# Performance work log

Hardware: AMD Instinct MI355X
Metric: run time of the kernel (lower is better)

The kernel has to match this reference:

```python
import jax, jax.numpy as jnp
import numpy as np

N_HEAD, D_MODEL, D_HEAD = 16, 1024, 64
QLEN, BSZ, RLEN = 2048, 2, 2048
SCALE = 1.0 / (D_HEAD ** 0.5)


def setup_inputs() -> dict:
    key = jax.random.key(0)
    ks = jax.random.split(key, 7)
    return {
        "w": jax.random.normal(ks[0], (QLEN, BSZ, D_MODEL), dtype=jnp.float32),
        "r": jax.random.normal(ks[1], (RLEN, D_MODEL), dtype=jnp.float32),
        "qkv_w": jax.random.normal(ks[2], (D_MODEL, 3 * N_HEAD * D_HEAD), dtype=jnp.float32) * 0.02,
        "r_net_w": jax.random.normal(ks[3], (D_MODEL, N_HEAD * D_HEAD), dtype=jnp.float32) * 0.02,
        "o_w": jax.random.normal(ks[4], (N_HEAD * D_HEAD, D_MODEL), dtype=jnp.float32) * 0.02,
        "r_r_bias": jax.random.normal(ks[5], (N_HEAD, D_HEAD), dtype=jnp.float32) * 0.02,
        "r_w_bias": jax.random.normal(ks[6], (N_HEAD, D_HEAD), dtype=jnp.float32) * 0.02,
    }


def _rel_shift(x):
    # x: [qlen, rlen, bsz, n_head]
    q, r, b, n = x.shape
    x = jnp.pad(x, ((0, 0), (1, 0), (0, 0), (0, 0)))
    x = x.reshape(r + 1, q, b, n)[1:]
    return x.reshape(q, r, b, n)


def reference(w, r, qkv_w, r_net_w, o_w, r_r_bias, r_w_bias):
    qlen, bsz, _ = w.shape
    rlen = r.shape[0]
    # qkv projection: [qlen, bsz, 3*H*D]
    w_heads = jnp.einsum('ibm,mh->ibh', w, qkv_w)
    w_head_q, w_head_k, w_head_v = jnp.split(w_heads, 3, axis=-1)
    klen = w_head_k.shape[0]
    w_head_q = w_head_q.reshape(qlen, bsz, N_HEAD, D_HEAD)
    w_head_k = w_head_k.reshape(klen, bsz, N_HEAD, D_HEAD)
    w_head_v = w_head_v.reshape(klen, bsz, N_HEAD, D_HEAD)
    # relative position keys: [rlen, H, D]
    r_head_k = jnp.einsum('jm,mh->jh', r, r_net_w).reshape(rlen, N_HEAD, D_HEAD)

    rw_head_q = w_head_q + r_w_bias  # content bias
    rr_head_q = w_head_q + r_r_bias  # position bias
    AC = jnp.einsum('ibnd,jbnd->ijbn', rw_head_q, w_head_k)
    BD = jnp.einsum('ibnd,jnd->ijbn', rr_head_q, r_head_k)
    BD = _rel_shift(BD)[:, :klen]

    attn_score = (AC + BD) * SCALE
    attn_prob = jax.nn.softmax(attn_score, axis=1)  # over klen axis
    attn_vec = jnp.einsum('ijbn,jbnd->ibnd', attn_prob, w_head_v)
    attn_vec = attn_vec.reshape(qlen, bsz, N_HEAD * D_HEAD)
    attn_out = jnp.einsum('ibh,hm->ibm', attn_vec, o_w)
    return (w + attn_out, attn_prob, AC, BD)
```

## Files before the change

kernel.cpp:

```cpp
#include <hip/hip_runtime.h>
#include <hip/hip_bf16.h>


typedef unsigned short u16;
typedef __attribute__((ext_vector_type(8))) short short8;
typedef __attribute__((ext_vector_type(4))) float f32x4;
typedef __attribute__((ext_vector_type(4))) unsigned short u16x4;

__device__ __forceinline__ u16 f2bf(float x){
  unsigned u = __float_as_uint(x);
  u += 0x7fffu + ((u >> 16) & 1u);
  return (u16)(u >> 16);
}
__device__ __forceinline__ float bf2f(u16 s){
  return __uint_as_float(((unsigned)s) << 16);
}
__device__ __forceinline__ f32x4 mfma16(short8 a, short8 b, f32x4 c){
  return __builtin_amdgcn_mfma_f32_16x16x32_bf16(a, b, c, 0, 0, 0);
}


__global__ __launch_bounds__(256) void k_cast(const float* __restrict__ src, u16* __restrict__ dst, int n4){
  int i = blockIdx.x * 256 + threadIdx.x;
  if (i >= n4) return;
  f32x4 v = *(const f32x4*)(src + (size_t)i * 4);
  u16x4 o;
  #pragma unroll
  for (int q = 0; q < 4; ++q) o[q] = f2bf(v[q]);
  *(u16x4*)(dst + (size_t)i * 4) = o;
}

__global__ __launch_bounds__(256) void k_tc(const float* __restrict__ src, u16* __restrict__ dst, int R, int C){
  __shared__ float ld[32][33];
  int c0 = blockIdx.x * 32, r0 = blockIdx.y * 32;
  int t = threadIdx.x;
  int r = t >> 3, c4 = (t & 7) * 4;
  f32x4 v = *(const f32x4*)(src + (size_t)(r0 + r) * C + c0 + c4);
  #pragma unroll
  for (int q = 0; q < 4; ++q) ld[r][c4 + q] = v[q];
  __syncthreads();
  int c = t >> 3, r4 = (t & 7) * 4;
  u16x4 o;
  #pragma unroll
  for (int q = 0; q < 4; ++q) o[q] = f2bf(ld[r4 + q][c]);
  *(u16x4*)(dst + (size_t)(c0 + c) * R + r0 + r4) = o;
}


template<int MODE>
__global__ __launch_bounds__(512) void k_gemm(const u16* __restrict__ A, const u16* __restrict__ Bt,
        u16* __restrict__ o0, u16* __restrict__ o1, u16* __restrict__ o2,
        const float* __restrict__ wres, float* __restrict__ outf)
{
  __shared__ __align__(16) u16 As[128][40];
  __shared__ __align__(16) u16 Bs[256][40];
  const int t = threadIdx.x;
  const int wave = t >> 6, lane = t & 63;
  const int wr = wave >> 2, wc = wave & 3;
  const int g = lane >> 4, li = lane & 15;
  const int m0 = blockIdx.x * 128, n0 = blockIdx.y * 256;
  f32x4 acc[4][4] = {};
  const int ar = t >> 2, ac8 = (t & 3) * 8;
  for (int kt = 0; kt < 32; ++kt){
    int k0 = kt * 32;
    *(short8*)&As[ar][ac8] = *(const short8*)(A + (size_t)(m0 + ar) * 1024 + k0 + ac8);
    #pragma unroll
    for (int u = 0; u < 2; ++u){
      int id = t + 512 * u; int br = id >> 2, bc8 = (id & 3) * 8;
      *(short8*)&Bs[br][bc8] = *(const short8*)(Bt + (size_t)(n0 + br) * 1024 + k0 + bc8);
    }
    __syncthreads();
    short8 af[4], bfv[4];
    #pragma unroll
    for (int mf = 0; mf < 4; ++mf) af[mf] = *(const short8*)&As[wr * 64 + mf * 16 + li][g * 8];
    #pragma unroll
    for (int nf = 0; nf < 4; ++nf) bfv[nf] = *(const short8*)&Bs[wc * 64 + nf * 16 + li][g * 8];
    #pragma unroll
    for (int mf = 0; mf < 4; ++mf)
      #pragma unroll
      for (int nf = 0; nf < 4; ++nf)
        acc[mf][nf] = mfma16(af[mf], bfv[nf], acc[mf][nf]);
    __syncthreads();
  }
  #pragma unroll
  for (int mf = 0; mf < 4; ++mf)
  #pragma unroll
  for (int nf = 0; nf < 4; ++nf)
  #pragma unroll
  for (int r = 0; r < 4; ++r){
    int gr = m0 + wr * 64 + mf * 16 + g * 4 + r;
    int gc = n0 + wc * 64 + nf * 16 + li;
    float v = acc[mf][nf][r];
    if (MODE == 0){
      int part = gc >> 10, hh = gc & 1023;
      int hn = hh >> 6, d = hh & 63;
      int i = gr >> 1, b = gr & 1;
      u16* dst = (part == 0) ? o0 : ((part == 1) ? o1 : o2);
      dst[((((b << 4) + hn) * 2048 + i) << 6) + d] = f2bf(v);
    } else if (MODE == 1){
      int hn = gc >> 6, d = gc & 63;
      o0[((hn * 2048 + gr) << 6) + d] = f2bf(v);
    } else {
      size_t idx = (size_t)gr * 1024 + gc;
      outf[idx] = wres[idx] + v;
    }
  }
}

__global__ __launch_bounds__(256) void k_bias(const u16* __restrict__ Km, const float* __restrict__ bv,
                                              float* __restrict__ out, int total){
  int idx = blockIdx.x * 256 + threadIdx.x;
  if (idx >= total) return;
  int n = (idx >> 11) & 15;
  const u16* kr = Km + ((size_t)idx << 6);
  const float* bp = bv + n * 64;
  float s = 0.f;
  #pragma unroll
  for (int d8 = 0; d8 < 8; ++d8){
    short8 v = *(const short8*)(kr + d8 * 8);
    #pragma unroll
    for (int q = 0; q < 8; ++q) s += bp[d8 * 8 + q] * bf2f((u16)v[q]);
  }
  out[idx] = s;
}

__global__ __launch_bounds__(256) void k_trv(const u16* __restrict__ V, u16* __restrict__ Vt){
  __shared__ __align__(16) u16 ld[64][72];
  int bn = blockIdx.x, j0 = blockIdx.y * 64;
  int t = threadIdx.x;
  #pragma unroll
  for (int u = 0; u < 2; ++u){
    int id = t + 256 * u; int r = id >> 3, c8 = (id & 7) * 8;
    *(short8*)&ld[r][c8] = *(const short8*)(V + ((size_t)(bn * 2048 + j0 + r) << 6) + c8);
  }
  __syncthreads();
  #pragma unroll
  for (int u = 0; u < 2; ++u){
    int id = t + 256 * u; int d = id >> 3, j8 = (id & 7) * 8;
    short8 o;
    #pragma unroll
    for (int q = 0; q < 8; ++q) o[q] = ld[j8 + q][d];
    *(short8*)(Vt + ((size_t)(bn * 64 + d) << 11) + j0 + j8) = o;
  }
}

__global__ __launch_bounds__(512, 4) void k_bd(const u16* __restrict__ Q, const u16* __restrict__ RK,
        const float* __restrict__ bias_bd, float* __restrict__ BD)
{
  __shared__ u16 Cs[32 * 271];
  const int t = threadIdx.x, wave = t >> 6, lane = t & 63;
  const int g = lane >> 4, li = lane & 15;
  const int i0 = blockIdx.x * 16, b = blockIdx.y;
  const int cbase = blockIdx.z * 512;
  short8 qa[2][2];
  #pragma unroll
  for (int nn = 0; nn < 2; ++nn){
    int bn = b * 16 + wave * 2 + nn;
    const u16* qp = Q + ((size_t)(bn * 2048 + i0 + li) << 6) + g * 8;
    qa[nn][0] = *(const short8*)qp;
    qa[nn][1] = *(const short8*)(qp + 32);
  }
  for (int ch = 0; ch < 16; ++ch){
    int c0 = cbase + ch * 32;
    #pragma unroll
    for (int nn = 0; nn < 2; ++nn){
      int n = wave * 2 + nn;
      #pragma unroll
      for (int cf = 0; cf < 2; ++cf){
        int ccol = c0 + cf * 16 + li;
        const u16* rp = RK + ((size_t)(n * 2048 + ccol) << 6) + g * 8;
        short8 b0 = *(const short8*)rp;
        short8 b1 = *(const short8*)(rp + 32);
        f32x4 acc = {};
        acc = mfma16(qa[nn][0], b0, acc);
        acc = mfma16(qa[nn][1], b1, acc);
        float bb = bias_bd[n * 2048 + ccol];
        #pragma unroll
        for (int r = 0; r < 4; ++r)
          Cs[(cf * 16 + li) * 271 + n * 17 + g * 4 + r] = f2bf(acc[r] + bb);
      }
    }
    __syncthreads();
    #pragma unroll
    for (int u = 0; u < 4; ++u){
      int flat4 = t + 512 * u;
      int n4 = (flat4 & 3) * 4, cl = (flat4 >> 2) & 31, row = flat4 >> 7;
      int ip = i0 + row, cg = c0 + cl;
      bool p1 = (cg >= 2047 - ip);
      int ro = p1 ? ip : (ip - 1);
      int j  = cg + (p1 ? (ip - 2047) : (ip + 1));
      if (ro >= 0){
        f32x4 v;
        #pragma unroll
        for (int q = 0; q < 4; ++q) v[q] = bf2f(Cs[cl * 271 + (n4 + q) * 17 + row]);
        *(f32x4*)(BD + (((size_t)ro * 2048 + j) << 5) + b * 16 + n4) = v;
      }
    }
    __syncthreads();
  }
}

__global__ __launch_bounds__(256) void k_bdiag(float* __restrict__ BD){
  int idx = blockIdx.x * 256 + threadIdx.x;
  int i = idx >> 5, c = idx & 31;
  if (i < 2047) BD[(((size_t)i * 2048 + i + 1) << 5) + c] = 0.f;
}

__global__ __launch_bounds__(512, 4) void k_stats(const u16* __restrict__ Q, const u16* __restrict__ Kc,
        const float* __restrict__ bias_ac, const float* __restrict__ BD,
        float* __restrict__ ACo, float* __restrict__ m_part, float* __restrict__ l_part)
{
  __shared__ float sA[16 * 545];
  __shared__ u16  sB[32 * 271];
  const int t = threadIdx.x, wave = t >> 6, lane = t & 63;
  const int g = lane >> 4, li = lane & 15;
  const int i0 = blockIdx.x * 16, b = blockIdx.y;
  const int jbase = blockIdx.z * 512;
  short8 qa[2][2];
  #pragma unroll
  for (int nn = 0; nn < 2; ++nn){
    int bn = b * 16 + wave * 2 + nn;
    const u16* qp = Q + ((size_t)(bn * 2048 + i0 + li) << 6) + g * 8;
    qa[nn][0] = *(const short8*)qp;
    qa[nn][1] = *(const short8*)(qp + 32);
  }
  float m_[2][4], l_[2][4];
  #pragma unroll
  for (int nn = 0; nn < 2; ++nn)
    #pragma unroll
    for (int r = 0; r < 4; ++r){ m_[nn][r] = -__builtin_inff(); l_[nn][r] = 0.f; }

  for (int ch = 0; ch < 16; ++ch){
    int j0 = jbase + ch * 32;
    __syncthreads();
    #pragma unroll
    for (int u = 0; u < 4; ++u){
      int flat4 = t + 512 * u;
      int n4 = (flat4 & 3) * 4, jl = (flat4 >> 2) & 31, row = flat4 >> 7;
      f32x4 v = *(const f32x4*)(BD + (((size_t)(i0 + row) * 2048 + j0 + jl) << 5) + b * 16 + n4);
      #pragma unroll
      for (int q = 0; q < 4; ++q) sA[row * 545 + jl * 17 + n4 + q] = v[q];
    }
    __syncthreads();
    #pragma unroll
    for (int nn = 0; nn < 2; ++nn){
      int n = wave * 2 + nn, bn = b * 16 + n;
      float sv[2][4];
      #pragma unroll
      for (int cf = 0; cf < 2; ++cf){
        int jc = j0 + cf * 16 + li;
        const u16* kp = Kc + ((size_t)(bn * 2048 + jc) << 6) + g * 8;
        short8 b0 = *(const short8*)kp;
        short8 b1 = *(const short8*)(kp + 32);
        f32x4 acc = {};
        acc = mfma16(qa[nn][0], b0, acc);
        acc = mfma16(qa[nn][1], b1, acc);
        float ba = bias_ac[bn * 2048 + jc];
        #pragma unroll
        for (int r = 0; r < 4; ++r){
          float av = acc[r] + ba;
          sB[(cf * 16 + li) * 271 + n * 17 + g * 4 + r] = f2bf(av);
          sv[cf][r] = (av + sA[(g * 4 + r) * 545 + (cf * 16 + li) * 17 + n]) * 0.125f;
        }
      }
      float cm[4], mn[4], ps[4];
      #pragma unroll
      for (int r = 0; r < 4; ++r) cm[r] = fmaxf(sv[0][r], sv[1][r]);
      #pragma unroll
      for (int off = 1; off < 16; off <<= 1)
        #pragma unroll
        for (int r = 0; r < 4; ++r) cm[r] = fmaxf(cm[r], __shfl_xor(cm[r], off));
      #pragma unroll
      for (int r = 0; r < 4; ++r){
        mn[r] = fmaxf(m_[nn][r], cm[r]);
        ps[r] = __expf(sv[0][r] - mn[r]) + __expf(sv[1][r] - mn[r]);
      }
      #pragma unroll
      for (int off = 1; off < 16; off <<= 1)
        #pragma unroll
        for (int r = 0; r < 4; ++r) ps[r] += __shfl_xor(ps[r], off);
      #pragma unroll
      for (int r = 0; r < 4; ++r){
        l_[nn][r] = l_[nn][r] * __expf(m_[nn][r] - mn[r]) + ps[r];
        m_[nn][r] = mn[r];
      }
    }
    __syncthreads();
    #pragma unroll
    for (int u = 0; u < 4; ++u){
      int flat4 = t + 512 * u;
      int n4 = (flat4 & 3) * 4, jl = (flat4 >> 2) & 31, row = flat4 >> 7;
      f32x4 v;
      #pragma unroll
      for (int q = 0; q < 4; ++q) v[q] = bf2f(sB[jl * 271 + (n4 + q) * 17 + row]);
      *(f32x4*)(ACo + (((size_t)(i0 + row) * 2048 + j0 + jl) << 5) + b * 16 + n4) = v;
    }
  }
  if (li == 0){
    #pragma unroll
    for (int nn = 0; nn < 2; ++nn)
      #pragma unroll
      for (int r = 0; r < 4; ++r){
        int bn = b * 16 + wave * 2 + nn;
        size_t o = ((size_t)(blockIdx.z * 32 + bn)) * 2048 + i0 + g * 4 + r;
        m_part[o] = m_[nn][r];
        l_part[o] = l_[nn][r];
      }
  }
}

__global__ __launch_bounds__(256) void k_comb(const float* __restrict__ mp, const float* __restrict__ lp,
                                              float* __restrict__ mf, float* __restrict__ lf){
  int idx = blockIdx.x * 256 + threadIdx.x;
  float m = -__builtin_inff();
  #pragma unroll
  for (int js = 0; js < 4; ++js) m = fmaxf(m, mp[js * 65536 + idx]);
  float l = 0.f;
  #pragma unroll
  for (int js = 0; js < 4; ++js) l += lp[js * 65536 + idx] * __expf(mp[js * 65536 + idx] - m);
  mf[idx] = m;
  lf[idx] = l;
}

__global__ __launch_bounds__(512, 4) void k_prob_pv(const u16* __restrict__ Q, const u16* __restrict__ Kc,
        const u16* __restrict__ Vt, const float* __restrict__ bias_ac, const float* __restrict__ BD,
        const float* __restrict__ m_f, const float* __restrict__ l_f,
        float* __restrict__ PROB, float* __restrict__ Ovp)
{
  __shared__ float sA[16 * 545];
  __shared__ u16  sB[32 * 271];
  const int t = threadIdx.x, wave = t >> 6, lane = t & 63;
  const int g = lane >> 4, li = lane & 15;
  const int i0 = blockIdx.x * 16, b = blockIdx.y;
  const int jbase = blockIdx.z * 512;
  short8 qa[2][2];
  float m_[2][4], rl_[2][4];
  #pragma unroll
  for (int nn = 0; nn < 2; ++nn){
    int bn = b * 16 + wave * 2 + nn;
    const u16* qp = Q + ((size_t)(bn * 2048 + i0 + li) << 6) + g * 8;
    qa[nn][0] = *(const short8*)qp;
    qa[nn][1] = *(const short8*)(qp + 32);
    #pragma unroll
    for (int r = 0; r < 4; ++r){
      m_[nn][r]  = m_f[bn * 2048 + i0 + g * 4 + r];
      rl_[nn][r] = 1.f / l_f[bn * 2048 + i0 + g * 4 + r];
    }
  }
  f32x4 oacc[2][4] = {};

  for (int ch = 0; ch < 16; ++ch){
    int j0 = jbase + ch * 32;
    __syncthreads();
    #pragma unroll
    for (int u = 0; u < 4; ++u){
      int flat4 = t + 512 * u;
      int n4 = (flat4 & 3) * 4, jl = (flat4 >> 2) & 31, row = flat4 >> 7;
      f32x4 v = *(const f32x4*)(BD + (((size_t)(i0 + row) * 2048 + j0 + jl) << 5) + b * 16 + n4);
      #pragma unroll
      for (int q = 0; q < 4; ++q) sA[row * 545 + jl * 17 + n4 + q] = v[q];
    }
    __syncthreads();
    #pragma unroll
    for (int nn = 0; nn < 2; ++nn){
      int n = wave * 2 + nn, bn = b * 16 + n;
      #pragma unroll
      for (int cf = 0; cf < 2; ++cf){
        int jc = j0 + cf * 16 + li;
        const u16* kp = Kc + ((size_t)(bn * 2048 + jc) << 6) + g * 8;
        short8 b0 = *(const short8*)kp;
        short8 b1 = *(const short8*)(kp + 32);
        f32x4 acc = {};
        acc = mfma16(qa[nn][0], b0, acc);
        acc = mfma16(qa[nn][1], b1, acc);
        float ba = bias_ac[bn * 2048 + jc];
        #pragma unroll
        for (int r = 0; r < 4; ++r){
          float s = (acc[r] + ba + sA[(g * 4 + r) * 545 + (cf * 16 + li) * 17 + n]) * 0.125f;
          float p = __expf(s - m_[nn][r]) * rl_[nn][r];
          sB[(cf * 16 + li) * 271 + n * 17 + g * 4 + r] = f2bf(p);
        }
      }
    }
    #pragma unroll
    for (int nn = 0; nn < 2; ++nn){
      int n = wave * 2 + nn, bn = b * 16 + n;
      short8 pa;
      #pragma unroll
      for (int tt = 0; tt < 8; ++tt) pa[tt] = (short)sB[(g * 8 + tt) * 271 + n * 17 + li];
      const u16* vb = Vt + ((size_t)(bn * 64) << 11) + j0 + g * 8;
      #pragma unroll
      for (int vf = 0; vf < 4; ++vf){
        short8 bv = *(const short8*)(vb + ((size_t)(vf * 16 + li) << 11));
        oacc[nn][vf] = mfma16(pa, bv, oacc[nn][vf]);
      }
    }
    __syncthreads();
    #pragma unroll
    for (int u = 0; u < 4; ++u){
      int flat4 = t + 512 * u;
      int n4 = (flat4 & 3) * 4, jl = (flat4 >> 2) & 31, row = flat4 >> 7;
      f32x4 v;
      #pragma unroll
      for (int q = 0; q < 4; ++q) v[q] = bf2f(sB[jl * 271 + (n4 + q) * 17 + row]);
      *(f32x4*)(PROB + (((size_t)(i0 + row) * 2048 + j0 + jl) << 5) + b * 16 + n4) = v;
    }
  }
  float* op = Ovp + (size_t)blockIdx.z * 4194304;
  #pragma unroll
  for (int nn = 0; nn < 2; ++nn){
    int n = wave * 2 + nn;
    #pragma unroll
    for (int vf = 0; vf < 4; ++vf)
      #pragma unroll
      for (int r = 0; r < 4; ++r)
        op[(size_t)((i0 + g * 4 + r) * 2 + b) * 1024 + n * 64 + vf * 16 + li] = oacc[nn][vf][r];
  }
}

__global__ __launch_bounds__(256) void k_ovred(const float* __restrict__ ovp, u16* __restrict__ ov){
  int i = blockIdx.x * 256 + threadIdx.x;
  const f32x4* p = (const f32x4*)ovp;
  f32x4 s = p[i];
  #pragma unroll
  for (int js = 1; js < 4; ++js) s += p[(size_t)js * 1048576 + i];
  u16x4 o;
  #pragma unroll
  for (int q = 0; q < 4; ++q) o[q] = f2bf(s[q]);
  ((u16x4*)ov)[i] = o;
}


extern "C" void kernel_launch(void* const* d_in, const int* in_sizes, int n_in,
                              void* d_out, int out_size, void* d_ws, size_t ws_size,
                              hipStream_t stream)
{
  const float* w      = (const float*)d_in[0];
  const float* r      = (const float*)d_in[1];
  const float* qkv_w  = (const float*)d_in[2];
  const float* rnet_w = (const float*)d_in[3];
  const float* o_w    = (const float*)d_in[4];
  const float* rrb    = (const float*)d_in[5];
  const float* rwb    = (const float*)d_in[6];

  char* ws = (char*)d_ws;
  size_t off = 0;
  auto alloc = [&](size_t bytes) -> void* {
    void* p = ws + off; off += (bytes + 255) & ~(size_t)255; return p;
  };
  u16* Xbf    = (u16*)alloc((size_t)4096 * 1024 * 2);
  u16* Rbf    = (u16*)alloc((size_t)2048 * 1024 * 2);
  u16* Wqkvt  = (u16*)alloc((size_t)3072 * 1024 * 2);
  u16* Wrt    = (u16*)alloc((size_t)1024 * 1024 * 2);
  u16* Wot    = (u16*)alloc((size_t)1024 * 1024 * 2);
  u16* Qs     = (u16*)alloc((size_t)32 * 2048 * 64 * 2);
  u16* Ks     = (u16*)alloc((size_t)32 * 2048 * 64 * 2);
  u16* Vs     = (u16*)alloc((size_t)32 * 2048 * 64 * 2);
  u16* Vts    = (u16*)alloc((size_t)32 * 64 * 2048 * 2);
  u16* RKs    = (u16*)alloc((size_t)16 * 2048 * 64 * 2);
  float* bias_ac = (float*)alloc((size_t)32 * 2048 * 4);
  float* bias_bd = (float*)alloc((size_t)16 * 2048 * 4);
  float* m_part  = (float*)alloc((size_t)4 * 32 * 2048 * 4);
  float* l_part  = (float*)alloc((size_t)4 * 32 * 2048 * 4);
  float* m_fin   = (float*)alloc((size_t)32 * 2048 * 4);
  float* l_fin   = (float*)alloc((size_t)32 * 2048 * 4);
  float* Ovp     = (float*)alloc((size_t)4 * 4096 * 1024 * 4);
  u16* Ov     = (u16*)alloc((size_t)4096 * 1024 * 2);

  float* out0 = (float*)d_out;
  float* PROB = out0 + 4194304;
  float* ACo  = PROB + 134217728;
  float* BDo  = ACo  + 134217728;

  k_cast<<<dim3(4096), dim3(256), 0, stream>>>(w, Xbf, 1048576);
  k_cast<<<dim3(2048), dim3(256), 0, stream>>>(r, Rbf, 524288);
  k_tc<<<dim3(96, 32), dim3(256), 0, stream>>>(qkv_w,  Wqkvt, 1024, 3072);
  k_tc<<<dim3(32, 32), dim3(256), 0, stream>>>(rnet_w, Wrt,   1024, 1024);
  k_tc<<<dim3(32, 32), dim3(256), 0, stream>>>(o_w,    Wot,   1024, 1024);
  k_gemm<0><<<dim3(32, 12), dim3(512), 0, stream>>>(Xbf, Wqkvt, Qs, Ks, Vs, nullptr, nullptr);
  k_gemm<1><<<dim3(16, 4),  dim3(512), 0, stream>>>(Rbf, Wrt,  RKs, nullptr, nullptr, nullptr, nullptr);
  k_bias<<<dim3(256), dim3(256), 0, stream>>>(Ks,  rwb, bias_ac, 65536);
  k_bias<<<dim3(128), dim3(256), 0, stream>>>(RKs, rrb, bias_bd, 32768);
  k_trv<<<dim3(32, 32), dim3(256), 0, stream>>>(Vs, Vts);
  k_bd<<<dim3(128, 2, 4), dim3(512), 0, stream>>>(Qs, RKs, bias_bd, BDo);
  k_bdiag<<<dim3(256), dim3(256), 0, stream>>>(BDo);
  k_stats<<<dim3(128, 2, 4), dim3(512), 0, stream>>>(Qs, Ks, bias_ac, BDo, ACo, m_part, l_part);
  k_comb<<<dim3(256), dim3(256), 0, stream>>>(m_part, l_part, m_fin, l_fin);
  k_prob_pv<<<dim3(128, 2, 4), dim3(512), 0, stream>>>(Qs, Ks, Vts, bias_ac, BDo, m_fin, l_fin, PROB, Ovp);
  k_ovred<<<dim3(4096), dim3(256), 0, stream>>>(Ovp, Ov);
  k_gemm<2><<<dim3(32, 4), dim3(512), 0, stream>>>(Ov, Wot, nullptr, nullptr, nullptr, w, out0);
}
```

Measured before the change: 1.375 ms.

## Fuse rel-shifted BD computation into stats and prob kernels, drop BD round trips

The separate BD kernel and diagonal-zero kernel are removed. The stats and prob/PV kernels now compute the rel-shifted BD tile on the fly: for each tile they run diagonal-band MFMAs with Q rows i and i+1 against the relevant RK columns and scatter the results into shared memory. This avoids writing BD to global memory and reading it back twice, which is 512MB of fp32 traffic. BD is still written once from the stats kernel, and all big outputs now use nontemporal stores. The cost is redundant BD MFMAs in both kernels, extra shared-memory clears each iteration, and BD values rounded to bf16 before they are added into the scores.

Result: slower. 1.614 ms (+17.4%).

```diff
diff --git a/kernel.cpp b/kernel.cpp
--- a/kernel.cpp
+++ b/kernel.cpp
@@ -17,6 +17,9 @@
 }
 __device__ __forceinline__ f32x4 mfma16(short8 a, short8 b, f32x4 c){
   return __builtin_amdgcn_mfma_f32_16x16x32_bf16(a, b, c, 0, 0, 0);
+}
+__device__ __forceinline__ void ntst4(float* p, f32x4 v){
+  __builtin_nontemporal_store(v, (f32x4*)p);
 }
 
 
@@ -144,86 +147,79 @@
   }
 }
 
-__global__ __launch_bounds__(512, 4) void k_bd(const u16* __restrict__ Q, const u16* __restrict__ RK,
-        const float* __restrict__ bias_bd, float* __restrict__ BD)
+__device__ __forceinline__ void bd_scatter(u16* sBD, const u16* __restrict__ RK,
+        const float* __restrict__ bias_bd, const short8 qa[2][2], const short8 qb[2][2],
+        int m, int wave, int g, int li)
 {
-  __shared__ u16 Cs[32 * 271];
+  #pragma unroll
+  for (int nn = 0; nn < 2; ++nn){
+    int n = wave * 2 + nn;
+    #pragma unroll
+    for (int tt = 0; tt < 3; ++tt){
+      int c0 = m + 2032 + tt * 16;
+      if (c0 < 0 || c0 > 2032) continue;
+      const u16* rp = RK + ((size_t)(n * 2048 + c0 + li) << 6) + g * 8;
+      short8 b0 = *(const short8*)rp;
+      short8 b1 = *(const short8*)(rp + 32);
+      f32x4 acc = {};
+      acc = mfma16(qa[nn][0], b0, acc);
+      acc = mfma16(qa[nn][1], b1, acc);
+      float bb = bias_bd[n * 2048 + c0 + li];
+      int off = tt * 16 - 15;
+      #pragma unroll
+      for (int r = 0; r < 4; ++r){
+        int fr = g * 4 + r;
+        int jw = li + fr + off;
+        if ((unsigned)jw < 32u) sBD[fr * 544 + jw * 17 + n] = f2bf(acc[r] + bb);
+      }
+    }
+    #pragma unroll
+    for (int tt = 0; tt < 4; ++tt){
+      int c0 = m - 32 + tt * 16;
+      if (c0 < 0 || c0 > 2032) continue;
+      const u16* rp = RK + ((size_t)(n * 2048 + c0 + li) << 6) + g * 8;
+      short8 b0 = *(const short8*)rp;
+      short8 b1 = *(const short8*)(rp + 32);
+      f32x4 acc = {};
+      acc = mfma16(qb[nn][0], b0, acc);
+      acc = mfma16(qb[nn][1], b1, acc);
+      float bb = bias_bd[n * 2048 + c0 + li];
+      int off = tt * 16 - 30;
+      #pragma unroll
+      for (int r = 0; r < 4; ++r){
+        int fr = g * 4 + r;
+        int jw = li + fr + off;
+        if ((unsigned)jw < 32u) sBD[fr * 544 + jw * 17 + n] = f2bf(acc[r] + bb);
+      }
+    }
+  }
+}
+
+__global__ __launch_bounds__(512, 4) void k_statsF(const u16* __restrict__ Q, const u16* __restrict__ RK,
+        const u16* __restrict__ Kc, const float* __restrict__ bias_ac, const float* __restrict__ bias_bd,
+        float* __restrict__ ACo, float* __restrict__ BDo,
+        float* __restrict__ m_part, float* __restrict__ l_part)
+{
+  __shared__ __align__(16) u16 sBD[16 * 544];
+  __shared__ __align__(16) u16 sAC[32 * 271];
   const int t = threadIdx.x, wave = t >> 6, lane = t & 63;
   const int g = lane >> 4, li = lane & 15;
   const int i0 = blockIdx.x * 16, b = blockIdx.y;
-  const int cbase = blockIdx.z * 512;
-  short8 qa[2][2];
+  const int jbase = blockIdx.z * 512;
+  short8 qa[2][2], qb[2][2];
   #pragma unroll
   for (int nn = 0; nn < 2; ++nn){
     int bn = b * 16 + wave * 2 + nn;
     const u16* qp = Q + ((size_t)(bn * 2048 + i0 + li) << 6) + g * 8;
     qa[nn][0] = *(const short8*)qp;
     qa[nn][1] = *(const short8*)(qp + 32);
-  }
-  for (int ch = 0; ch < 16; ++ch){
-    int c0 = cbase + ch * 32;
-    #pragma unroll
-    for (int nn = 0; nn < 2; ++nn){
-      int n = wave * 2 + nn;
-      #pragma unroll
-      for (int cf = 0; cf < 2; ++cf){
-        int ccol = c0 + cf * 16 + li;
-        const u16* rp = RK + ((size_t)(n * 2048 + ccol) << 6) + g * 8;
-        short8 b0 = *(const short8*)rp;
-        short8 b1 = *(const short8*)(rp + 32);
-        f32x4 acc = {};
-        acc = mfma16(qa[nn][0], b0, acc);
-        acc = mfma16(qa[nn][1], b1, acc);
-        float bb = bias_bd[n * 2048 + ccol];
-        #pragma unroll
-        for (int r = 0; r < 4; ++r)
-          Cs[(cf * 16 + li) * 271 + n * 17 + g * 4 + r] = f2bf(acc[r] + bb);
-      }
-    }
-    __syncthreads();
-    #pragma unroll
-    for (int u = 0; u < 4; ++u){
-      int flat4 = t + 512 * u;
-      int n4 = (flat4 & 3) * 4, cl = (flat4 >> 2) & 31, row = flat4 >> 7;
-      int ip = i0 + row, cg = c0 + cl;
-      bool p1 = (cg >= 2047 - ip);
-      int ro = p1 ? ip : (ip - 1);
-      int j  = cg + (p1 ? (ip - 2047) : (ip + 1));
-      if (ro >= 0){
-        f32x4 v;
-        #pragma unroll
-        for (int q = 0; q < 4; ++q) v[q] = bf2f(Cs[cl * 271 + (n4 + q) * 17 + row]);
-        *(f32x4*)(BD + (((size_t)ro * 2048 + j) << 5) + b * 16 + n4) = v;
-      }
-    }
-    __syncthreads();
-  }
-}
-
-__global__ __launch_bounds__(256) void k_bdiag(float* __restrict__ BD){
-  int idx = blockIdx.x * 256 + threadIdx.x;
-  int i = idx >> 5, c = idx & 31;
-  if (i < 2047) BD[(((size_t)i * 2048 + i + 1) << 5) + c] = 0.f;
-}
-
-__global__ __launch_bounds__(512, 4) void k_stats(const u16* __restrict__ Q, const u16* __restrict__ Kc,
-        const float* __restrict__ bias_ac, const float* __restrict__ BD,
-        float* __restrict__ ACo, float* __restrict__ m_part, float* __restrict__ l_part)
-{
-  __shared__ float sA[16 * 545];
-  __shared__ u16  sB[32 * 271];
-  const int t = threadIdx.x, wave = t >> 6, lane = t & 63;
-  const int g = lane >> 4, li = lane & 15;
-  const int i0 = blockIdx.x * 16, b = blockIdx.y;
-  const int jbase = blockIdx.z * 512;
-  short8 qa[2][2];
-  #pragma unroll
-  for (int nn = 0; nn < 2; ++nn){
-    int bn = b * 16 + wave * 2 + nn;
-    const u16* qp = Q + ((size_t)(bn * 2048 + i0 + li) << 6) + g * 8;
-    qa[nn][0] = *(const short8*)qp;
-    qa[nn][1] = *(const short8*)(qp + 32);
-  }
+    int rowB = i0 + 1 + li; if (rowB > 2047) rowB = 2047;
+    const u16* qp2 = Q + ((size_t)(bn * 2048 + rowB) << 6) + g * 8;
+    qb[nn][0] = *(const short8*)qp2;
+    qb[nn][1] = *(const short8*)(qp2 + 32);
+  }
+  for (int w = t; w < 4352; w += 512) ((unsigned*)sBD)[w] = 0;
+
   float m_[2][4], l_[2][4];
   #pragma unroll
   for (int nn = 0; nn < 2; ++nn)
@@ -232,15 +228,9 @@
 
   for (int ch = 0; ch < 16; ++ch){
     int j0 = jbase + ch * 32;
-    __syncthreads();
-    #pragma unroll
-    for (int u = 0; u < 4; ++u){
-      int flat4 = t + 512 * u;
-      int n4 = (flat4 & 3) * 4, jl = (flat4 >> 2) & 31, row = flat4 >> 7;
-      f32x4 v = *(const f32x4*)(BD + (((size_t)(i0 + row) * 2048 + j0 + jl) << 5) + b * 16 + n4);
-      #pragma unroll
-      for (int q = 0; q < 4; ++q) sA[row * 545 + jl * 17 + n4 + q] = v[q];
-    }
+    int m = j0 - i0;
+    __syncthreads();
+    bd_scatter(sBD, RK, bias_bd, qa, qb, m, wave, g, li);
     __syncthreads();
     #pragma unroll
     for (int nn = 0; nn < 2; ++nn){
@@ -259,8 +249,9 @@
         #pragma unroll
         for (int r = 0; r < 4; ++r){
           float av = acc[r] + ba;
-          sB[(cf * 16 + li) * 271 + n * 17 + g * 4 + r] = f2bf(av);
-          sv[cf][r] = (av + sA[(g * 4 + r) * 545 + (cf * 16 + li) * 17 + n]) * 0.125f;
+          sAC[(cf * 16 + li) * 271 + n * 17 + g * 4 + r] = f2bf(av);
+          float bd = bf2f(sBD[(g * 4 + r) * 544 + (cf * 16 + li) * 17 + n]);
+          sv[cf][r] = (av + bd) * 0.125f;
         }
       }
       float cm[4], mn[4], ps[4];
@@ -285,16 +276,26 @@
         m_[nn][r] = mn[r];
       }
     }
-    __syncthreads();
     #pragma unroll
     for (int u = 0; u < 4; ++u){
       int flat4 = t + 512 * u;
       int n4 = (flat4 & 3) * 4, jl = (flat4 >> 2) & 31, row = flat4 >> 7;
       f32x4 v;
       #pragma unroll
-      for (int q = 0; q < 4; ++q) v[q] = bf2f(sB[jl * 271 + (n4 + q) * 17 + row]);
-      *(f32x4*)(ACo + (((size_t)(i0 + row) * 2048 + j0 + jl) << 5) + b * 16 + n4) = v;
-    }
+      for (int q = 0; q < 4; ++q) v[q] = bf2f(sBD[row * 544 + jl * 17 + n4 + q]);
+      ntst4(BDo + (((size_t)(i0 + row) * 2048 + j0 + jl) << 5) + b * 16 + n4, v);
+    }
+    __syncthreads();
+    #pragma unroll
+    for (int u = 0; u < 4; ++u){
+      int flat4 = t + 512 * u;
+      int n4 = (flat4 & 3) * 4, jl = (flat4 >> 2) & 31, row = flat4 >> 7;
+      f32x4 v;
+      #pragma unroll
+      for (int q = 0; q < 4; ++q) v[q] = bf2f(sAC[jl * 271 + (n4 + q) * 17 + row]);
+      ntst4(ACo + (((size_t)(i0 + row) * 2048 + j0 + jl) << 5) + b * 16 + n4, v);
+    }
+    for (int w = t; w < 4352; w += 512) ((unsigned*)sBD)[w] = 0;
   }
   if (li == 0){
     #pragma unroll
@@ -322,13 +323,14 @@
   lf[idx] = l;
 }
 
-__global__ __launch_bounds__(512, 4) void k_prob_pv(const u16* __restrict__ Q, const u16* __restrict__ Kc,
-        const u16* __restrict__ Vt, const float* __restrict__ bias_ac, const float* __restrict__ BD,
+__global__ __launch_bounds__(512, 4) void k_probF(const u16* __restrict__ Q, const u16* __restrict__ RK,
+        const u16* __restrict__ Kc, const u16* __restrict__ Vt,
+        const float* __restrict__ bias_ac, const float* __restrict__ bias_bd,
         const float* __restrict__ m_f, const float* __restrict__ l_f,
         float* __restrict__ PROB, float* __restrict__ Ovp)
 {
-  __shared__ float sA[16 * 545];
-  __shared__ u16  sB[32 * 271];
+  __shared__ __align__(16) u16 sBD[16 * 544];
+  __shared__ __align__(16) u16 sP[32 * 271];
   const int t = threadIdx.x, wave = t >> 6, lane = t & 63;
   const int g = lane >> 4, li = lane & 15;
   const int i0 = blockIdx.x * 16, b = blockIdx.y;
@@ -347,18 +349,24 @@
       rl_[nn][r] = 1.f / l_f[bn * 2048 + i0 + g * 4 + r];
     }
   }
+  for (int w = t; w < 4352; w += 512) ((unsigned*)sBD)[w] = 0;
   f32x4 oacc[2][4] = {};
 
   for (int ch = 0; ch < 16; ++ch){
     int j0 = jbase + ch * 32;
-    __syncthreads();
-    #pragma unroll
-    for (int u = 0; u < 4; ++u){
-      int flat4 = t + 512 * u;
-      int n4 = (flat4 & 3) * 4, jl = (flat4 >> 2) & 31, row = flat4 >> 7;
-      f32x4 v = *(const f32x4*)(BD + (((size_t)(i0 + row) * 2048 + j0 + jl) << 5) + b * 16 + n4);
-      #pragma unroll
-      for (int q = 0; q < 4; ++q) sA[row * 545 + jl * 17 + n4 + q] = v[q];
+    int m = j0 - i0;
+    __syncthreads();
+    {
+      short8 qb[2][2];
+      #pragma unroll
+      for (int nn = 0; nn < 2; ++nn){
+        int bn = b * 16 + wave * 2 + nn;
+        int rowB = i0 + 1 + li; if (rowB > 2047) rowB = 2047;
+        const u16* qp2 = Q + ((size_t)(bn * 2048 + rowB) << 6) + g * 8;
+        qb[nn][0] = *(const short8*)qp2;
+        qb[nn][1] = *(const short8*)(qp2 + 32);
+      }
+      bd_scatter(sBD, RK, bias_bd, qa, qb, m, wave, g, li);
     }
     __syncthreads();
     #pragma unroll
@@ -376,9 +384,10 @@
         float ba = bias_ac[bn * 2048 + jc];
         #pragma unroll
         for (int r = 0; r < 4; ++r){
-          float s = (acc[r] + ba + sA[(g * 4 + r) * 545 + (cf * 16 + li) * 17 + n]) * 0.125f;
+          float bd = bf2f(sBD[(g * 4 + r) * 544 + (cf * 16 + li) * 17 + n]);
+          float s = (acc[r] + ba + bd) * 0.125f;
           float p = __expf(s - m_[nn][r]) * rl_[nn][r];
-          sB[(cf * 16 + li) * 271 + n * 17 + g * 4 + r] = f2bf(p);
+          sP[(cf * 16 + li) * 271 + n * 17 + g * 4 + r] = f2bf(p);
         }
       }
     }
@@ -387,7 +396,7 @@
       int n = wave * 2 + nn, bn = b * 16 + n;
       short8 pa;
       #pragma unroll
-      for (int tt = 0; tt < 8; ++tt) pa[tt] = (short)sB[(g * 8 + tt) * 271 + n * 17 + li];
+      for (int tt = 0; tt < 8; ++tt) pa[tt] = (short)sP[(g * 8 + tt) * 271 + n * 17 + li];
       const u16* vb = Vt + ((size_t)(bn * 64) << 11) + j0 + g * 8;
       #pragma unroll
       for (int vf = 0; vf < 4; ++vf){
@@ -402,9 +411,10 @@
       int n4 = (flat4 & 3) * 4, jl = (flat4 >> 2) & 31, row = flat4 >> 7;
       f32x4 v;
       #pragma unroll
-      for (int q = 0; q < 4; ++q) v[q] = bf2f(sB[jl * 271 + (n4 + q) * 17 + row]);
-      *(f32x4*)(PROB + (((size_t)(i0 + row) * 2048 + j0 + jl) << 5) + b * 16 + n4) = v;
-    }
+      for (int q = 0; q < 4; ++q) v[q] = bf2f(sP[jl * 271 + (n4 + q) * 17 + row]);
+      ntst4(PROB + (((size_t)(i0 + row) * 2048 + j0 + jl) << 5) + b * 16 + n4, v);
+    }
+    for (int w = t; w < 4352; w += 512) ((unsigned*)sBD)[w] = 0;
   }
   float* op = Ovp + (size_t)blockIdx.z * 4194304;
   #pragma unroll
@@ -482,11 +492,9 @@
   k_bias<<<dim3(256), dim3(256), 0, stream>>>(Ks,  rwb, bias_ac, 65536);
   k_bias<<<dim3(128), dim3(256), 0, stream>>>(RKs, rrb, bias_bd, 32768);
   k_trv<<<dim3(32, 32), dim3(256), 0, stream>>>(Vs, Vts);
-  k_bd<<<dim3(128, 2, 4), dim3(512), 0, stream>>>(Qs, RKs, bias_bd, BDo);
-  k_bdiag<<<dim3(256), dim3(256), 0, stream>>>(BDo);
-  k_stats<<<dim3(128, 2, 4), dim3(512), 0, stream>>>(Qs, Ks, bias_ac, BDo, ACo, m_part, l_part);
+  k_statsF<<<dim3(128, 2, 4), dim3(512), 0, stream>>>(Qs, RKs, Ks, bias_ac, bias_bd, ACo, BDo, m_part, l_part);
   k_comb<<<dim3(256), dim3(256), 0, stream>>>(m_part, l_part, m_fin, l_fin);
-  k_prob_pv<<<dim3(128, 2, 4), dim3(512), 0, stream>>>(Qs, Ks, Vts, bias_ac, BDo, m_fin, l_fin, PROB, Ovp);
+  k_probF<<<dim3(128, 2, 4), dim3(512), 0, stream>>>(Qs, RKs, Ks, Vts, bias_ac, bias_bd, m_fin, l_fin, PROB, Ovp);
   k_ovred<<<dim3(4096), dim3(256), 0, stream>>>(Ovp, Ov);
   k_gemm<2><<<dim3(32, 4), dim3(512), 0, stream>>>(Ov, Wot, nullptr, nullptr, nullptr, w, out0);
 }
```

## Prefetch BD tiles into registers, store BD in LDS as bf16, use nontemporal stores

Applied to the files above, without the earlier changes.

The stats and prob/PV kernels now prefetch the next chunk's BD tile into registers while the current chunk is being processed, so global load latency overlaps compute. The BD tile is staged in shared memory as truncated bf16 with a padded vectorized layout, which cuts LDS size and store traffic. The large BD, AC and PROB output writes use nontemporal stores so these streams do not pollute the cache. The risks are extra register pressure from the prefetch buffers and the precision lost by truncating BD to bf16 in the score calculation.

After: 1.257 ms. -8.5%, faster.

```diff
diff --git a/kernel.cpp b/kernel.cpp
--- a/kernel.cpp
+++ b/kernel.cpp
@@ -17,6 +17,9 @@
 }
 __device__ __forceinline__ f32x4 mfma16(short8 a, short8 b, f32x4 c){
   return __builtin_amdgcn_mfma_f32_16x16x32_bf16(a, b, c, 0, 0, 0);
+}
+__device__ __forceinline__ void ntst4(float* p, f32x4 v){
+  __builtin_nontemporal_store(v, (f32x4*)p);
 }
 
 
@@ -193,7 +196,7 @@
         f32x4 v;
         #pragma unroll
         for (int q = 0; q < 4; ++q) v[q] = bf2f(Cs[cl * 271 + (n4 + q) * 17 + row]);
-        *(f32x4*)(BD + (((size_t)ro * 2048 + j) << 5) + b * 16 + n4) = v;
+        ntst4(BD + (((size_t)ro * 2048 + j) << 5) + b * 16 + n4, v);
       }
     }
     __syncthreads();
@@ -210,8 +213,8 @@
         const float* __restrict__ bias_ac, const float* __restrict__ BD,
         float* __restrict__ ACo, float* __restrict__ m_part, float* __restrict__ l_part)
 {
-  __shared__ float sA[16 * 545];
-  __shared__ u16  sB[32 * 271];
+  __shared__ __align__(16) u16 sA[16 * 648];
+  __shared__ u16 sB[32 * 271];
   const int t = threadIdx.x, wave = t >> 6, lane = t & 63;
   const int g = lane >> 4, li = lane & 15;
   const int i0 = blockIdx.x * 16, b = blockIdx.y;
@@ -230,6 +233,14 @@
     #pragma unroll
     for (int r = 0; r < 4; ++r){ m_[nn][r] = -__builtin_inff(); l_[nn][r] = 0.f; }
 
+  f32x4 pfv[4];
+  #pragma unroll
+  for (int u = 0; u < 4; ++u){
+    int flat4 = t + 512 * u;
+    int n4 = (flat4 & 3) * 4, jl = (flat4 >> 2) & 31, row = flat4 >> 7;
+    pfv[u] = *(const f32x4*)(BD + (((size_t)(i0 + row) * 2048 + jbase + jl) << 5) + b * 16 + n4);
+  }
+
   for (int ch = 0; ch < 16; ++ch){
     int j0 = jbase + ch * 32;
     __syncthreads();
@@ -237,9 +248,18 @@
     for (int u = 0; u < 4; ++u){
       int flat4 = t + 512 * u;
       int n4 = (flat4 & 3) * 4, jl = (flat4 >> 2) & 31, row = flat4 >> 7;
-      f32x4 v = *(const f32x4*)(BD + (((size_t)(i0 + row) * 2048 + j0 + jl) << 5) + b * 16 + n4);
-      #pragma unroll
-      for (int q = 0; q < 4; ++q) sA[row * 545 + jl * 17 + n4 + q] = v[q];
+      u16x4 o;
+      #pragma unroll
+      for (int q = 0; q < 4; ++q) o[q] = (u16)(__float_as_uint(pfv[u][q]) >> 16);
+      *(u16x4*)&sA[row * 648 + jl * 20 + n4] = o;
+    }
+    if (ch + 1 < 16){
+      #pragma unroll
+      for (int u = 0; u < 4; ++u){
+        int flat4 = t + 512 * u;
+        int n4 = (flat4 & 3) * 4, jl = (flat4 >> 2) & 31, row = flat4 >> 7;
+        pfv[u] = *(const f32x4*)(BD + (((size_t)(i0 + row) * 2048 + j0 + 32 + jl) << 5) + b * 16 + n4);
+      }
     }
     __syncthreads();
     #pragma unroll
@@ -260,7 +280,8 @@
         for (int r = 0; r < 4; ++r){
           float av = acc[r] + ba;
           sB[(cf * 16 + li) * 271 + n * 17 + g * 4 + r] = f2bf(av);
-          sv[cf][r] = (av + sA[(g * 4 + r) * 545 + (cf * 16 + li) * 17 + n]) * 0.125f;
+          float bd = bf2f(sA[(g * 4 + r) * 648 + (cf * 16 + li) * 20 + n]);
+          sv[cf][r] = (av + bd) * 0.125f;
         }
       }
       float cm[4], mn[4], ps[4];
@@ -293,7 +314,7 @@
       f32x4 v;
       #pragma unroll
       for (int q = 0; q < 4; ++q) v[q] = bf2f(sB[jl * 271 + (n4 + q) * 17 + row]);
-      *(f32x4*)(ACo + (((size_t)(i0 + row) * 2048 + j0 + jl) << 5) + b * 16 + n4) = v;
+      ntst4(ACo + (((size_t)(i0 + row) * 2048 + j0 + jl) << 5) + b * 16 + n4, v);
     }
   }
   if (li == 0){
@@ -327,8 +348,8 @@
         const float* __restrict__ m_f, const float* __restrict__ l_f,
         float* __restrict__ PROB, float* __restrict__ Ovp)
 {
-  __shared__ float sA[16 * 545];
-  __shared__ u16  sB[32 * 271];
+  __shared__ __align__(16) u16 sA[16 * 648];
+  __shared__ u16 sB[32 * 271];
   const int t = threadIdx.x, wave = t >> 6, lane = t & 63;
   const int g = lane >> 4, li = lane & 15;
   const int i0 = blockIdx.x * 16, b = blockIdx.y;
@@ -349,6 +370,14 @@
   }
   f32x4 oacc[2][4] = {};
 
+  f32x4 pfv[4];
+  #pragma unroll
+  for (int u = 0; u < 4; ++u){
+    int flat4 = t + 512 * u;
+    int n4 = (flat4 & 3) * 4, jl = (flat4 >> 2) & 31, row = flat4 >> 7;
+    pfv[u] = *(const f32x4*)(BD + (((size_t)(i0 + row) * 2048 + jbase + jl) << 5) + b * 16 + n4);
+  }
+
   for (int ch = 0; ch < 16; ++ch){
     int j0 = jbase + ch * 32;
     __syncthreads();
@@ -356,9 +385,18 @@
     for (int u = 0; u < 4; ++u){
       int flat4 = t + 512 * u;
       int n4 = (flat4 & 3) * 4, jl = (flat4 >> 2) & 31, row = flat4 >> 7;
-      f32x4 v = *(const f32x4*)(BD + (((size_t)(i0 + row) * 2048 + j0 + jl) << 5) + b * 16 + n4);
-      #pragma unroll
-      for (int q = 0; q < 4; ++q) sA[row * 545 + jl * 17 + n4 + q] = v[q];
+      u16x4 o;
+      #pragma unroll
+      for (int q = 0; q < 4; ++q) o[q] = (u16)(__float_as_uint(pfv[u][q]) >> 16);
+      *(u16x4*)&sA[row * 648 + jl * 20 + n4] = o;
+    }
+    if (ch + 1 < 16){
+      #pragma unroll
+      for (int u = 0; u < 4; ++u){
+        int flat4 = t + 512 * u;
+        int n4 = (flat4 & 3) * 4, jl = (flat4 >> 2) & 31, row = flat4 >> 7;
+        pfv[u] = *(const f32x4*)(BD + (((size_t)(i0 + row) * 2048 + j0 + 32 + jl) << 5) + b * 16 + n4);
+      }
     }
     __syncthreads();
     #pragma unroll
@@ -376,7 +414,8 @@
         float ba = bias_ac[bn * 2048 + jc];
         #pragma unroll
         for (int r = 0; r < 4; ++r){
-          float s = (acc[r] + ba + sA[(g * 4 + r) * 545 + (cf * 16 + li) * 17 + n]) * 0.125f;
+          float bd = bf2f(sA[(g * 4 + r) * 648 + (cf * 16 + li) * 20 + n]);
+          float s = (acc[r] + ba + bd) * 0.125f;
           float p = __expf(s - m_[nn][r]) * rl_[nn][r];
           sB[(cf * 16 + li) * 271 + n * 17 + g * 4 + r] = f2bf(p);
         }
@@ -403,7 +442,7 @@
       f32x4 v;
       #pragma unroll
       for (int q = 0; q < 4; ++q) v[q] = bf2f(sB[jl * 271 + (n4 + q) * 17 + row]);
-      *(f32x4*)(PROB + (((size_t)(i0 + row) * 2048 + j0 + jl) << 5) + b * 16 + n4) = v;
+      ntst4(PROB + (((size_t)(i0 + row) * 2048 + j0 + jl) << 5) + b * 16 + n4, v);
     }
   }
   float* op = Ovp + (size_t)blockIdx.z * 4194304;
```
